# Kernel optimization log

Hardware: AMD Instinct MI355X
Metric: run time of the kernel (lower is better)

## Reference

```python
import jax, jax.numpy as jnp
import numpy as np
import math

B, L = 2048, 60
D, H, NL = 80, 8, 3
HD = D // H            # head_dim = 10
NLOC, NUSR = 1187, 46
DFF = 2 * D
IN_DIM = D + 24 + 32 + 2   # loc(80)+user(24)+weekday(16)+hour(16)+2 continuous


def _ln(x, g, b):
    m = jnp.mean(x, -1, keepdims=True)
    v = jnp.mean((x - m) ** 2, -1, keepdims=True)
    return (x - m) * jax.lax.rsqrt(v + 1e-5) * g + b


def setup_inputs():
    key = jax.random.key(0)
    k = lambda i: jax.random.fold_in(key, i)
    g = lambda i, shp, s: jax.random.normal(k(i), shp, dtype=jnp.float32) * s
    inp = {
        "loc_seq": jax.random.randint(k(0), (B, L), 0, NLOC),
        "user_seq": jax.random.randint(k(1), (B, L), 0, NUSR),
        "weekday_seq": jax.random.randint(k(2), (B, L), 0, 8),
        "start_min_seq": jax.random.randint(k(3), (B, L), 0, 1440),
        "dur_seq": jax.random.randint(k(4), (B, L), 0, 600),
        "diff_seq": jax.random.randint(k(5), (B, L), 0, 100),
        "seq_len": jax.random.randint(k(6), (B,), 1, L + 1),
    }
    # embedding tables (padding_idx=0 rows zeroed where the module uses it)
    inp["loc_table"] = g(10, (NLOC, D), 0.02).at[0].set(0.0)
    inp["user_table"] = g(11, (NUSR, 24), 0.02).at[0].set(0.0)
    inp["wk_table"] = g(12, (8, 16), 0.02).at[0].set(0.0)
    inp["hr_table"] = g(13, (25, 16), 0.02)
    inp["in_w"] = g(14, (IN_DIM, D), 0.09)
    inp["in_b"] = jnp.zeros((D,), jnp.float32)
    inp["in_g"] = jnp.ones((D,), jnp.float32)
    inp["in_be"] = jnp.zeros((D,), jnp.float32)
    inp["pos_emb"] = g(15, (1, L, D), 0.02)
    # per-layer stacked params (NL=3 layers)
    inp["qkv_w"] = g(16, (NL, D, 3 * D), 0.09)
    inp["proj_w"] = g(17, (NL, D, D), 0.11)
    inp["proj_b"] = jnp.zeros((NL, D), jnp.float32)
    inp["rel_emb"] = g(18, (NL, 2 * L - 1, HD), 1.0)
    inp["n1_g"] = jnp.ones((NL, D), jnp.float32)
    inp["n1_b"] = jnp.zeros((NL, D), jnp.float32)
    inp["ffn_w1"] = g(19, (NL, D, DFF), 0.09)
    inp["ffn_b1"] = jnp.zeros((NL, DFF), jnp.float32)
    inp["ffn_w2"] = g(20, (NL, DFF, D), 0.09)
    inp["ffn_b2"] = jnp.zeros((NL, D), jnp.float32)
    inp["n2_g"] = jnp.ones((NL, D), jnp.float32)
    inp["n2_b"] = jnp.zeros((NL, D), jnp.float32)
    inp["fn_g"] = jnp.ones((D,), jnp.float32)
    inp["fn_b"] = jnp.zeros((D,), jnp.float32)
    inp["pr_w1"] = g(21, (D, D), 0.11)
    inp["pr_b1"] = jnp.zeros((D,), jnp.float32)
    inp["pr_w2"] = g(22, (D, NLOC), 0.04)
    inp["pr_b2"] = jnp.zeros((NLOC,), jnp.float32)
    inp["protos"] = g(23, (NLOC, D), 0.04)
    inp["temp"] = jnp.asarray(2.0, jnp.float32)
    return inp


def reference(loc_seq, user_seq, weekday_seq, start_min_seq, dur_seq, diff_seq, seq_len,
              loc_table, user_table, wk_table, hr_table, in_w, in_b, in_g, in_be, pos_emb,
              qkv_w, proj_w, proj_b, rel_emb, n1_g, n1_b, ffn_w1, ffn_b1, ffn_w2, ffn_b2,
              n2_g, n2_b, fn_g, fn_b, pr_w1, pr_b1, pr_w2, pr_b2, protos, temp):
    Bx, Lx = loc_seq.shape
    loc_e = loc_table[loc_seq]                                            # [B,L,80]
    user_e = jnp.broadcast_to(user_table[user_seq[:, 0]][:, None, :], (Bx, Lx, 24))
    hour = jnp.clip(start_min_seq // 60, 0, 23)
    cont = jnp.stack([diff_seq.astype(jnp.float32) / 10.0,
                      dur_seq.astype(jnp.float32) / 300.0], -1)           # [B,L,2]
    x = jnp.concatenate([loc_e, user_e, wk_table[weekday_seq], hr_table[hour], cont], -1)
    x = _ln(x @ in_w + in_b, in_g, in_be) + pos_emb[:, :Lx, :]
    key_mask = loc_seq == 0                                               # mask keys [B,L]
    pos_idx = jnp.arange(Lx)[None, :] - jnp.arange(Lx)[:, None] + (Lx - 1)  # [L,L]
    scale = 1.0 / math.sqrt(HD)
    for l in range(NL):
        qkv = (x @ qkv_w[l]).reshape(Bx, Lx, 3, H, HD)
        q = qkv[:, :, 0].transpose(0, 2, 1, 3)                            # [B,H,L,hd]
        kk = qkv[:, :, 1].transpose(0, 2, 1, 3)
        v = qkv[:, :, 2].transpose(0, 2, 1, 3)
        rel = rel_emb[l][pos_idx]                                         # [L,L,hd]
        attn = (jnp.einsum('bhid,bhjd->bhij', q, kk)
                + jnp.einsum('bhid,ijd->bhij', q, rel)) * scale
        attn = jnp.where(key_mask[:, None, None, :], -jnp.inf, attn)
        a = jax.nn.softmax(attn, -1)
        o = jnp.einsum('bhij,bhjd->bhid', a, v).transpose(0, 2, 1, 3).reshape(Bx, Lx, D)
        x = _ln(x + o @ proj_w[l] + proj_b[l], n1_g[l], n1_b[l])
        f = jax.nn.gelu(x @ ffn_w1[l] + ffn_b1[l], approximate=False) @ ffn_w2[l] + ffn_b2[l]
        x = _ln(x + f, n2_g[l], n2_b[l])
    x = _ln(x, fn_g, fn_b)
    final = x[jnp.arange(Bx), jnp.clip(seq_len - 1, 0, Lx - 1)]           # [B,80]
    logits_param = jax.nn.gelu(final @ pr_w1 + pr_b1, approximate=False) @ pr_w2 + pr_b2
    fnorm = final / jnp.maximum(jnp.linalg.norm(final, axis=-1, keepdims=True), 1e-12)
    pnorm = protos / jnp.maximum(jnp.linalg.norm(protos, axis=-1, keepdims=True), 1e-12)
    logits = 0.5 * logits_param + 0.5 * (fnorm @ pnorm.T) * 15.0
    return logits / jnp.clip(temp, 0.5, 3.0)
```

## Files before the change

### kernel.cpp

```cpp
#include <hip/hip_runtime.h>
#include <hip/hip_bf16.h>
#include <math.h>

#define BB   2048
#define LL   60
#define DD   80
#define HH   8
#define HDD  10
#define NLNUM 3
#define NLOC 1187
#define DFF  160
#define IN_DIM 138
#define RELN 119
#define SCS  68
#define XP   21
#define HP   41
#define VP   35
#define TS   65

__device__ __forceinline__ float gelu_f(float a) {
  float x = fabsf(a) * 0.70710678118654752f;
  float t = 1.0f / (1.0f + 0.3275911f * x);
  float y = t * (0.254829592f + t * (-0.284496736f + t * (1.421413741f +
            t * (-1.453152027f + t * 1.061405429f))));
  float e = 1.0f - y * __expf(-x * x);
  float erf_s = copysignf(e, a);
  return 0.5f * a * (1.0f + erf_s);
}

__global__ __launch_bounds__(256) void k_rprep(
    const float* __restrict__ rel_emb, float* __restrict__ relTg) {
  int idx = blockIdx.x * 256 + threadIdx.x;
  if (idx >= 3600) return;
  int p = idx % 120;
  int d = (idx / 120) % 10;
  int l = idx / 1200;
  float v = 0.0f;
  if (p < RELN) v = rel_emb[l * RELN * HDD + p * HDD + d];
  relTg[idx] = v;
}

__global__ __launch_bounds__(256) void k_embed(
    const int* __restrict__ loc_seq, const int* __restrict__ user_seq,
    const int* __restrict__ wk_seq, const int* __restrict__ sm_seq,
    const int* __restrict__ dur_seq, const int* __restrict__ diff_seq,
    const float* __restrict__ loc_table, const float* __restrict__ user_table,
    const float* __restrict__ wk_table, const float* __restrict__ hr_table,
    const float* __restrict__ in_w, const float* __restrict__ in_b,
    const float* __restrict__ in_g, const float* __restrict__ in_be,
    const float* __restrict__ pos_emb, float* __restrict__ x) {
  int tok0 = blockIdx.x * 48, tid = threadIdx.x;
  __shared__ __align__(16) float vin[48 * VP * 4];
  __shared__ __align__(16) float ws[140 * 80];
  __shared__ float mstd[96];

  float4* vin4 = (float4*)vin;
  float4* ws4  = (float4*)ws;

  for (int i = tid; i < 140 * 20; i += 256) {
    int r = i / 20, c = i % 20;
    float4 v = make_float4(0.0f, 0.0f, 0.0f, 0.0f);
    if (r < IN_DIM) v = *(const float4*)(in_w + r * 80 + c * 4);
    ws4[i] = v;
  }
  for (int i = tid; i < 48 * 35; i += 256) {
    int t = i / 35, s = i % 35;
    int tok = tok0 + t;
    float4 v;
    if (s < 20) {
      int loc = loc_seq[tok];
      v = *(const float4*)(loc_table + (size_t)loc * 80 + s * 4);
    } else if (s < 26) {
      int usr = user_seq[(tok / LL) * LL];
      v = *(const float4*)(user_table + usr * 24 + (s - 20) * 4);
    } else if (s < 30) {
      int wk = wk_seq[tok];
      v = *(const float4*)(wk_table + wk * 16 + (s - 26) * 4);
    } else if (s < 34) {
      int hr = sm_seq[tok] / 60; hr = min(max(hr, 0), 23);
      v = *(const float4*)(hr_table + hr * 16 + (s - 30) * 4);
    } else {
      v.x = (float)diff_seq[tok] / 10.0f;
      v.y = (float)dur_seq[tok] / 300.0f;
      v.z = 0.0f; v.w = 0.0f;
    }
    vin4[t * VP + s] = v;
  }
  __syncthreads();

  int tg = tid / 20, cg = tid % 20, t0 = tg * 4;
  float acc[4][4] = {};
  if (tid < 240) {
    #pragma unroll 7
    for (int iq = 0; iq < 35; iq++) {
      float4 xv[4], wv[4];
      #pragma unroll
      for (int dt = 0; dt < 4; dt++) xv[dt] = vin4[(t0 + dt) * VP + iq];
      #pragma unroll
      for (int di = 0; di < 4; di++) wv[di] = ws4[(iq * 4 + di) * 20 + cg];
      #pragma unroll
      for (int dt = 0; dt < 4; dt++) {
        const float* xp = (const float*)&xv[dt];
        #pragma unroll
        for (int di = 0; di < 4; di++) {
          const float* wp = (const float*)&wv[di];
          #pragma unroll
          for (int dc = 0; dc < 4; dc++) acc[dt][dc] += xp[di] * wp[dc];
        }
      }
    }
  }
  __syncthreads();
  if (tid < 240) {
    float4 bb = *(const float4*)(in_b + cg * 4);
    const float* bp = (const float*)&bb;
    #pragma unroll
    for (int dt = 0; dt < 4; dt++) {
      float4 y;
      y.x = acc[dt][0] + bp[0];
      y.y = acc[dt][1] + bp[1];
      y.z = acc[dt][2] + bp[2];
      y.w = acc[dt][3] + bp[3];
      vin4[(t0 + dt) * VP + cg] = y;
    }
  }
  __syncthreads();
  if (tid < 48) {
    float s = 0.0f, s2 = 0.0f;
    #pragma unroll
    for (int iq = 0; iq < 20; iq++) {
      float4 v = vin4[tid * VP + iq];
      s  += v.x + v.y + v.z + v.w;
      s2 += v.x * v.x + v.y * v.y + v.z * v.z + v.w * v.w;
    }
    float mean = s / 80.0f;
    float var  = fmaxf(s2 / 80.0f - mean * mean, 0.0f);
    mstd[tid] = mean; mstd[48 + tid] = rsqrtf(var + 1e-5f);
  }
  __syncthreads();
  for (int e = tid; e < 960; e += 256) {
    int t = e / 20, c4 = e % 20;
    float4 v = vin4[t * VP + c4];
    float4 gg = *(const float4*)(in_g + c4 * 4);
    float4 bb = *(const float4*)(in_be + c4 * 4);
    float4 pe = *(const float4*)(pos_emb + ((tok0 + t) % LL) * 80 + c4 * 4);
    float m = mstd[t], r = mstd[48 + t];
    float4 out;
    out.x = (v.x - m) * r * gg.x + bb.x + pe.x;
    out.y = (v.y - m) * r * gg.y + bb.y + pe.y;
    out.z = (v.z - m) * r * gg.z + bb.z + pe.z;
    out.w = (v.w - m) * r * gg.w + bb.w + pe.w;
    ((float4*)(x + (size_t)tok0 * 80))[e] = out;
  }
}

__global__ __launch_bounds__(256) void k_qkv(
    const float* __restrict__ x, const float* __restrict__ qkv_w,
    float* __restrict__ qkvo) {
  int b = blockIdx.x, tid = threadIdx.x;
  __shared__ __align__(16) float xsT[20 * TS * 4];
  __shared__ __align__(16) float ws[80 * 60];

  const float4* xb4 = (const float4*)(x + (size_t)b * 4800);
  float4* xsT4 = (float4*)xsT;
  float4* ws4  = (float4*)ws;
  for (int i = tid; i < 1200; i += 256) {
    int t = i / 20, iq = i % 20;
    xsT4[iq * TS + t] = xb4[i];
  }

  for (int c0 = 0; c0 < 240; c0 += 60) {
    __syncthreads();
    for (int i = tid; i < 1200; i += 256)
      ws4[i] = *(const float4*)(qkv_w + (i / 15) * 240 + c0 + (i % 15) * 4);
    __syncthreads();
    if (tid < 225) {
      int tg = tid % 15, cg = tid / 15;
      int t0 = tg * 4;
      float acc[4][4] = {};
      #pragma unroll 5
      for (int iq = 0; iq < 20; iq++) {
        float4 xv[4], wv[4];
        #pragma unroll
        for (int dt = 0; dt < 4; dt++) xv[dt] = xsT4[iq * TS + t0 + dt];
        #pragma unroll
        for (int di = 0; di < 4; di++) wv[di] = ws4[(iq * 4 + di) * 15 + cg];
        #pragma unroll
        for (int dt = 0; dt < 4; dt++) {
          const float* xp = (const float*)&xv[dt];
          #pragma unroll
          for (int di = 0; di < 4; di++) {
            const float* wp = (const float*)&wv[di];
            #pragma unroll
            for (int dc = 0; dc < 4; dc++) acc[dt][dc] += xp[di] * wp[dc];
          }
        }
      }
      float* qb = qkvo + (size_t)b * 14400 + (size_t)(c0 + cg * 4) * 60 + t0;
      #pragma unroll
      for (int dc = 0; dc < 4; dc++)
        *(float4*)(qb + dc * 60) =
            make_float4(acc[0][dc], acc[1][dc], acc[2][dc], acc[3][dc]);
    }
  }
}

__global__ __launch_bounds__(256) void k_attn(
    const float* __restrict__ qkvo, const int* __restrict__ loc_seq,
    const float* __restrict__ relTg,
    float* __restrict__ o) {
  int bh = blockIdx.x;
  int b = bh >> 3, h = bh & 7;
  int tid = threadIdx.x;

  __shared__ __align__(16) float qs[HDD * 60];
  __shared__ __align__(16) float ks[HDD * 60];
  __shared__ __align__(16) float vs[HDD * 60];
  __shared__ __align__(16) float relT[HDD * 120];
  __shared__ __align__(16) float sc[60 * SCS];
  __shared__ __align__(16) float rsum[64];
  __shared__ float msk[60];

  const float4* src = (const float4*)(qkvo + (size_t)b * 14400);
  float4* q4 = (float4*)qs; float4* k4 = (float4*)ks; float4* v4 = (float4*)vs;
  for (int i = tid; i < 150; i += 256) {
    q4[i] = src[h * 150 + i];
    k4[i] = src[1200 + h * 150 + i];
    v4[i] = src[2400 + h * 150 + i];
  }
  const float4* rg4 = (const float4*)relTg;
  float4* relT4 = (float4*)relT;
  for (int i = tid; i < 300; i += 256) relT4[i] = rg4[i];
  if (tid < 60) msk[tid] = (loc_seq[b * LL + tid] == 0) ? 1.0f : 0.0f;
  __syncthreads();

  if (tid < 225) {
    int ig = tid / 15, jg = tid % 15;
    int i0 = ig * 4, j0 = jg * 4;
    int w0 = j0 - i0 + 56;
    float acc[4][4] = {};
    #pragma unroll
    for (int d = 0; d < 10; d++) {
      float4 qv = *(const float4*)(qs + d * 60 + i0);
      float4 kv = *(const float4*)(ks + d * 60 + j0);
      float4 rA = *(const float4*)(relT + d * 120 + w0);
      float4 rB = *(const float4*)(relT + d * 120 + w0 + 4);
      float rr[8] = {rA.x, rA.y, rA.z, rA.w, rB.x, rB.y, rB.z, rB.w};
      const float* qp = (const float*)&qv;
      const float* kp = (const float*)&kv;
      #pragma unroll
      for (int di = 0; di < 4; di++)
        #pragma unroll
        for (int dj = 0; dj < 4; dj++)
          acc[di][dj] += qp[di] * (kp[dj] + rr[dj - di + 3]);
    }
    const float scale = 0.31622776601683794f;
    #pragma unroll
    for (int di = 0; di < 4; di++) {
      #pragma unroll
      for (int dj = 0; dj < 4; dj++) {
        float v = acc[di][dj] * scale;
        if (msk[j0 + dj] != 0.0f) v = -1e30f;
        acc[di][dj] = v;
      }
      *(float4*)(sc + (i0 + di) * SCS + j0) =
          make_float4(acc[di][0], acc[di][1], acc[di][2], acc[di][3]);
    }
  }
  __syncthreads();

  if (tid < 60) {
    float* row = sc + tid * SCS;
    int c = (tid >> 3) & 7;
    float m0 = -3.0e38f, m1 = -3.0e38f, m2 = -3.0e38f, m3 = -3.0e38f;
    #pragma unroll
    for (int s = 0; s < 15; s++) {
      int k = c + s; if (k >= 15) k -= 15;
      float4 v = *(const float4*)(row + 4 * k);
      m0 = fmaxf(m0, v.x); m1 = fmaxf(m1, v.y);
      m2 = fmaxf(m2, v.z); m3 = fmaxf(m3, v.w);
    }
    float m = fmaxf(fmaxf(m0, m1), fmaxf(m2, m3));
    float s0 = 0.0f, s1 = 0.0f, s2 = 0.0f, s3 = 0.0f;
    #pragma unroll
    for (int s = 0; s < 15; s++) {
      int k = c + s; if (k >= 15) k -= 15;
      float4 v = *(float4*)(row + 4 * k);
      v.x = __expf(v.x - m); v.y = __expf(v.y - m);
      v.z = __expf(v.z - m); v.w = __expf(v.w - m);
      *(float4*)(row + 4 * k) = v;
      s0 += v.x; s1 += v.y; s2 += v.z; s3 += v.w;
    }
    rsum[tid] = 1.0f / (s0 + s1 + s2 + s3);
  }
  __syncthreads();

  if (tid < 150) {
    int ig = tid / 10, d = tid % 10;
    float acc[4] = {0, 0, 0, 0};
    #pragma unroll 5
    for (int jq = 0; jq < 15; jq++) {
      float4 vv = *(const float4*)(vs + d * 60 + jq * 4);
      #pragma unroll
      for (int di = 0; di < 4; di++) {
        float4 av = *(const float4*)(sc + (ig + 15 * di) * SCS + jq * 4);
        acc[di] += av.x * vv.x + av.y * vv.y + av.z * vv.z + av.w * vv.w;
      }
    }
    #pragma unroll
    for (int di = 0; di < 4; di++) {
      float r = rsum[ig + 15 * di];
      o[((size_t)b * 60 + ig + 15 * di) * 80 + h * 10 + d] = acc[di] * r;
    }
  }
}

__global__ __launch_bounds__(256) void k_pffn(
    const float* __restrict__ o, const float* __restrict__ proj_w,
    const float* __restrict__ proj_b, const float* __restrict__ g1,
    const float* __restrict__ be1,
    const float* __restrict__ w1, const float* __restrict__ b1,
    const float* __restrict__ w2, const float* __restrict__ b2,
    const float* __restrict__ g2, const float* __restrict__ be2,
    float* __restrict__ x) {
  int tok0 = blockIdx.x * 48, tid = threadIdx.x;
  __shared__ __align__(16) float ys[48 * XP * 4];
  __shared__ __align__(16) float hs[48 * HP * 4];
  __shared__ __align__(16) float ws[80 * 80];
  __shared__ float mstd[96];

  float4* ys4 = (float4*)ys;
  float4* hs4 = (float4*)hs;
  float4* os4 = (float4*)hs;
  float4* ws4 = (float4*)ws;

  const float4* ob4 = (const float4*)(o + (size_t)tok0 * 80);
  for (int i = tid; i < 960; i += 256) os4[(i / 20) * XP + (i % 20)] = ob4[i];
  for (int i = tid; i < 1600; i += 256)
    ws4[i] = *(const float4*)(proj_w + (i / 20) * 80 + (i % 20) * 4);
  __syncthreads();

  int tg = tid / 20, cg = tid % 20, t0 = tg * 4;
  {
    float acc[4][4] = {};
    if (tid < 240) {
      #pragma unroll
      for (int iq = 0; iq < 20; iq++) {
        float4 xv[4], wv[4];
        #pragma unroll
        for (int dt = 0; dt < 4; dt++) xv[dt] = os4[(t0 + dt) * XP + iq];
        #pragma unroll
        for (int di = 0; di < 4; di++) wv[di] = ws4[(iq * 4 + di) * 20 + cg];
        #pragma unroll
        for (int dt = 0; dt < 4; dt++) {
          const float* xp = (const float*)&xv[dt];
          #pragma unroll
          for (int di = 0; di < 4; di++) {
            const float* wp = (const float*)&wv[di];
            #pragma unroll
            for (int dc = 0; dc < 4; dc++) acc[dt][dc] += xp[di] * wp[dc];
          }
        }
      }
      float4 pb = *(const float4*)(proj_b + cg * 4);
      const float* pbp = (const float*)&pb;
      #pragma unroll
      for (int dt = 0; dt < 4; dt++) {
        float4 xr = *(const float4*)(x + (size_t)(tok0 + t0 + dt) * 80 + cg * 4);
        const float* xrp = (const float*)&xr;
        float4 out;
        out.x = acc[dt][0] + pbp[0] + xrp[0];
        out.y = acc[dt][1] + pbp[1] + xrp[1];
        out.z = acc[dt][2] + pbp[2] + xrp[2];
        out.w = acc[dt][3] + pbp[3] + xrp[3];
        ys4[(t0 + dt) * XP + cg] = out;
      }
    }
  }
  __syncthreads();
  if (tid < 48) {
    float s = 0.0f, s2 = 0.0f;
    #pragma unroll
    for (int iq = 0; iq < 20; iq++) {
      float4 v = ys4[tid * XP + iq];
      s  += v.x + v.y + v.z + v.w;
      s2 += v.x * v.x + v.y * v.y + v.z * v.z + v.w * v.w;
    }
    float mean = s / 80.0f;
    float var  = fmaxf(s2 / 80.0f - mean * mean, 0.0f);
    mstd[tid] = mean; mstd[48 + tid] = rsqrtf(var + 1e-5f);
  }
  __syncthreads();
  for (int e = tid; e < 960; e += 256) {
    int t = e / 20, c4 = e % 20;
    float4 v = ys4[t * XP + c4];
    float4 gg = *(const float4*)(g1 + c4 * 4);
    float4 bb = *(const float4*)(be1 + c4 * 4);
    float m = mstd[t], r = mstd[48 + t];
    v.x = (v.x - m) * r * gg.x + bb.x;
    v.y = (v.y - m) * r * gg.y + bb.y;
    v.z = (v.z - m) * r * gg.z + bb.z;
    v.w = (v.w - m) * r * gg.w + bb.w;
    ys4[t * XP + c4] = v;
  }

  for (int c0 = 0; c0 < 160; c0 += 80) {
    __syncthreads();
    for (int i = tid; i < 1600; i += 256)
      ws4[i] = *(const float4*)(w1 + (i / 20) * 160 + c0 + (i % 20) * 4);
    __syncthreads();
    if (tid < 240) {
      float acc[4][4] = {};
      #pragma unroll
      for (int iq = 0; iq < 20; iq++) {
        float4 xv[4], wv[4];
        #pragma unroll
        for (int dt = 0; dt < 4; dt++) xv[dt] = ys4[(t0 + dt) * XP + iq];
        #pragma unroll
        for (int di = 0; di < 4; di++) wv[di] = ws4[(iq * 4 + di) * 20 + cg];
        #pragma unroll
        for (int dt = 0; dt < 4; dt++) {
          const float* xp = (const float*)&xv[dt];
          #pragma unroll
          for (int di = 0; di < 4; di++) {
            const float* wp = (const float*)&wv[di];
            #pragma unroll
            for (int dc = 0; dc < 4; dc++) acc[dt][dc] += xp[di] * wp[dc];
          }
        }
      }
      float4 bb = *(const float4*)(b1 + c0 + cg * 4);
      const float* bp = (const float*)&bb;
      #pragma unroll
      for (int dt = 0; dt < 4; dt++) {
        float4 out;
        float* op = (float*)&out;
        #pragma unroll
        for (int dc = 0; dc < 4; dc++)
          op[dc] = gelu_f(acc[dt][dc] + bp[dc]);
        hs4[(t0 + dt) * HP + c0 / 4 + cg] = out;
      }
    }
  }

  float acc[4][4] = {};
  for (int k0 = 0; k0 < 160; k0 += 80) {
    __syncthreads();
    for (int i = tid; i < 1600; i += 256)
      ws4[i] = *(const float4*)(w2 + (size_t)(k0 + i / 20) * 80 + (i % 20) * 4);
    __syncthreads();
    if (tid < 240) {
      #pragma unroll
      for (int iq = 0; iq < 20; iq++) {
        float4 hv[4], wv[4];
        #pragma unroll
        for (int dt = 0; dt < 4; dt++) hv[dt] = hs4[(t0 + dt) * HP + k0 / 4 + iq];
        #pragma unroll
        for (int di = 0; di < 4; di++) wv[di] = ws4[(iq * 4 + di) * 20 + cg];
        #pragma unroll
        for (int dt = 0; dt < 4; dt++) {
          const float* hp = (const float*)&hv[dt];
          #pragma unroll
          for (int di = 0; di < 4; di++) {
            const float* wp = (const float*)&wv[di];
            #pragma unroll
            for (int dc = 0; dc < 4; dc++) acc[dt][dc] += hp[di] * wp[dc];
          }
        }
      }
    }
  }
  __syncthreads();
  if (tid < 240) {
    float4 bb = *(const float4*)(b2 + cg * 4);
    const float* bp = (const float*)&bb;
    #pragma unroll
    for (int dt = 0; dt < 4; dt++) {
      float4 xr = ys4[(t0 + dt) * XP + cg];
      const float* xrp = (const float*)&xr;
      float4 out;
      out.x = acc[dt][0] + bp[0] + xrp[0];
      out.y = acc[dt][1] + bp[1] + xrp[1];
      out.z = acc[dt][2] + bp[2] + xrp[2];
      out.w = acc[dt][3] + bp[3] + xrp[3];
      hs4[(t0 + dt) * HP + cg] = out;
    }
  }
  __syncthreads();
  if (tid < 48) {
    float s = 0.0f, s2 = 0.0f;
    #pragma unroll
    for (int iq = 0; iq < 20; iq++) {
      float4 v = hs4[tid * HP + iq];
      s  += v.x + v.y + v.z + v.w;
      s2 += v.x * v.x + v.y * v.y + v.z * v.z + v.w * v.w;
    }
    float mean = s / 80.0f;
    float var  = fmaxf(s2 / 80.0f - mean * mean, 0.0f);
    mstd[tid] = mean; mstd[48 + tid] = rsqrtf(var + 1e-5f);
  }
  __syncthreads();
  for (int e = tid; e < 960; e += 256) {
    int t = e / 20, c4 = e % 20;
    float4 v = hs4[t * HP + c4];
    float4 gg = *(const float4*)(g2 + c4 * 4);
    float4 bb = *(const float4*)(be2 + c4 * 4);
    float m = mstd[t], r = mstd[48 + t];
    float4 out;
    out.x = (v.x - m) * r * gg.x + bb.x;
    out.y = (v.y - m) * r * gg.y + bb.y;
    out.z = (v.z - m) * r * gg.z + bb.z;
    out.w = (v.w - m) * r * gg.w + bb.w;
    ((float4*)(x + (size_t)tok0 * 80))[e] = out;
  }
}

__global__ __launch_bounds__(128) void k_final(
    const float* __restrict__ x, const int* __restrict__ seq_len,
    const float* __restrict__ fn_g, const float* __restrict__ fn_b,
    const float* __restrict__ pr_w1, const float* __restrict__ pr_b1,
    float* __restrict__ fnorm, float* __restrict__ h1) {
  int b = blockIdx.x, tid = threadIdx.x;
  __shared__ float red[128], red2[128];
  __shared__ float fbuf[DD];
  int t = seq_len[b] - 1; t = min(max(t, 0), LL - 1);
  float v = 0.0f;
  if (tid < DD) v = x[((size_t)b * LL + t) * DD + tid];
  red[tid]  = (tid < DD) ? v : 0.0f;
  red2[tid] = (tid < DD) ? v * v : 0.0f;
  __syncthreads();
  for (int s = 64; s > 0; s >>= 1) {
    if (tid < s) { red[tid] += red[tid + s]; red2[tid] += red2[tid + s]; }
    __syncthreads();
  }
  float mean = red[0] / DD;
  float var  = fmaxf(red2[0] / DD - mean * mean, 0.0f);
  float rstd = rsqrtf(var + 1e-5f);
  float f = 0.0f;
  if (tid < DD) { f = (v - mean) * rstd * fn_g[tid] + fn_b[tid]; fbuf[tid] = f; }
  __syncthreads();
  red[tid] = (tid < DD) ? f * f : 0.0f;
  __syncthreads();
  for (int s = 64; s > 0; s >>= 1) {
    if (tid < s) red[tid] += red[tid + s];
    __syncthreads();
  }
  float rn = 1.0f / fmaxf(sqrtf(red[0]), 1e-12f);
  if (tid < DD) {
    fnorm[(size_t)b * DD + tid] = f * rn;
    float gacc = pr_b1[tid];
    for (int i = 0; i < DD; i++) gacc += fbuf[i] * pr_w1[i * DD + tid];
    h1[(size_t)b * DD + tid] = gelu_f(gacc);
  }
}

__global__ __launch_bounds__(128) void k_pnorm(
    const float* __restrict__ protos, float* __restrict__ pnormT) {
  int c = blockIdx.x, tid = threadIdx.x;
  __shared__ float red[128];
  float v = 0.0f;
  if (tid < DD) v = protos[(size_t)c * DD + tid];
  red[tid] = (tid < DD) ? v * v : 0.0f;
  __syncthreads();
  for (int s = 64; s > 0; s >>= 1) {
    if (tid < s) red[tid] += red[tid + s];
    __syncthreads();
  }
  float rn = 1.0f / fmaxf(sqrtf(red[0]), 1e-12f);
  if (tid < DD) pnormT[(size_t)tid * NLOC + c] = v * rn;
}

__global__ __launch_bounds__(256) void k_logits(
    const float* __restrict__ h1, const float* __restrict__ fnorm,
    const float* __restrict__ pr_w2, const float* __restrict__ pr_b2,
    const float* __restrict__ pnormT, const float* __restrict__ temp,
    float* __restrict__ out) {
  int b0 = (blockIdx.x / 5) * 4, cb = blockIdx.x % 5;
  int tid = threadIdx.x;
  int c = cb * 256 + tid;
  __shared__ float h1s[4][DD], fns[4][DD];
  for (int i = tid; i < 4 * DD; i += 256) {
    int j = i / DD, k = i % DD;
    h1s[j][k] = h1[(size_t)(b0 + j) * DD + k];
    fns[j][k] = fnorm[(size_t)(b0 + j) * DD + k];
  }
  __syncthreads();
  if (c < NLOC) {
    float a1[4] = {0, 0, 0, 0}, a2[4] = {0, 0, 0, 0};
    for (int k = 0; k < DD; k++) {
      float w = pr_w2[(size_t)k * NLOC + c];
      float p = pnormT[(size_t)k * NLOC + c];
      #pragma unroll
      for (int j = 0; j < 4; j++) {
        a1[j] += h1s[j][k] * w;
        a2[j] += fns[j][k] * p;
      }
    }
    float pb = pr_b2[c];
    float tt = fminf(fmaxf(temp[0], 0.5f), 3.0f);
    #pragma unroll
    for (int j = 0; j < 4; j++)
      out[(size_t)(b0 + j) * NLOC + c] = (0.5f * (a1[j] + pb) + 7.5f * a2[j]) / tt;
  }
}

extern "C" void kernel_launch(void* const* d_in, const int* in_sizes, int n_in,
                              void* d_out, int out_size, void* d_ws, size_t ws_size,
                              hipStream_t stream) {
  const int* loc_seq   = (const int*)d_in[0];
  const int* user_seq  = (const int*)d_in[1];
  const int* wk_seq    = (const int*)d_in[2];
  const int* sm_seq    = (const int*)d_in[3];
  const int* dur_seq   = (const int*)d_in[4];
  const int* diff_seq  = (const int*)d_in[5];
  const int* seq_len   = (const int*)d_in[6];
  const float* loc_table = (const float*)d_in[7];
  const float* user_table= (const float*)d_in[8];
  const float* wk_table  = (const float*)d_in[9];
  const float* hr_table  = (const float*)d_in[10];
  const float* in_w   = (const float*)d_in[11];
  const float* in_b   = (const float*)d_in[12];
  const float* in_g   = (const float*)d_in[13];
  const float* in_be  = (const float*)d_in[14];
  const float* pos_emb= (const float*)d_in[15];
  const float* qkv_w  = (const float*)d_in[16];
  const float* proj_w = (const float*)d_in[17];
  const float* proj_b = (const float*)d_in[18];
  const float* rel_emb= (const float*)d_in[19];
  const float* n1_g   = (const float*)d_in[20];
  const float* n1_b   = (const float*)d_in[21];
  const float* ffn_w1 = (const float*)d_in[22];
  const float* ffn_b1 = (const float*)d_in[23];
  const float* ffn_w2 = (const float*)d_in[24];
  const float* ffn_b2 = (const float*)d_in[25];
  const float* n2_g   = (const float*)d_in[26];
  const float* n2_b   = (const float*)d_in[27];
  const float* fn_g   = (const float*)d_in[28];
  const float* fn_b   = (const float*)d_in[29];
  const float* pr_w1  = (const float*)d_in[30];
  const float* pr_b1  = (const float*)d_in[31];
  const float* pr_w2  = (const float*)d_in[32];
  const float* pr_b2  = (const float*)d_in[33];
  const float* protos = (const float*)d_in[34];
  const float* temp   = (const float*)d_in[35];
  float* out = (float*)d_out;

  float* x      = (float*)d_ws;
  float* o      = x + (size_t)BB * LL * DD;
  float* qkvo   = o + (size_t)BB * LL * DD;
  float* fnorm  = qkvo + (size_t)BB * 14400;
  float* h1     = fnorm + (size_t)BB * DD;
  float* pnormT = h1 + (size_t)BB * DD;
  float* relTg  = pnormT + (size_t)DD * NLOC;

  k_rprep<<<15, 256, 0, stream>>>(rel_emb, relTg);

  k_embed<<<BB * LL / 48, 256, 0, stream>>>(loc_seq, user_seq, wk_seq, sm_seq,
                                            dur_seq, diff_seq, loc_table,
                                            user_table, wk_table, hr_table,
                                            in_w, in_b, in_g, in_be, pos_emb, x);

  for (int l = 0; l < NLNUM; l++) {
    k_qkv<<<BB, 256, 0, stream>>>(x, qkv_w + (size_t)l * 80 * 240, qkvo);
    k_attn<<<BB * HH, 256, 0, stream>>>(qkvo, loc_seq,
                                        relTg + (size_t)l * 1200, o);
    k_pffn<<<BB * LL / 48, 256, 0, stream>>>(
        o, proj_w + (size_t)l * DD * DD, proj_b + (size_t)l * DD,
        n1_g + (size_t)l * DD, n1_b + (size_t)l * DD,
        ffn_w1 + (size_t)l * DD * DFF, ffn_b1 + (size_t)l * DFF,
        ffn_w2 + (size_t)l * DFF * DD, ffn_b2 + (size_t)l * DD,
        n2_g + (size_t)l * DD, n2_b + (size_t)l * DD, x);
  }

  k_pnorm<<<NLOC, 128, 0, stream>>>(protos, pnormT);
  k_final<<<BB, 128, 0, stream>>>(x, seq_len, fn_g, fn_b, pr_w1, pr_b1, fnorm, h1);
  k_logits<<<(BB / 4) * 5, 256, 0, stream>>>(h1, fnorm, pr_w2, pr_b2, pnormT, temp, out);
}
```

Measured before the change: 1.520 ms.

## Switch embed, QKV and FFN kernels to one-token-per-thread register GEMMs

Rewrites k_embed, k_qkv and k_pffn so each thread owns one token and keeps its full 80-wide row in registers. Weights are read directly from global memory with uniform (broadcast) indices instead of being staged through shared memory, which removes all __syncthreads and the LDS tiling. Launch grids change to 256 tokens per block, or 4 batches per block for QKV. The cost is very high register pressure from 80-160 float arrays, which risks spills and low occupancy. Every thread also redundantly streams the whole weight matrix through the scalar/L1 path, and the strided per-thread stores in k_qkv are uncoalesced.

```diff
diff --git a/kernel.cpp b/kernel.cpp
--- a/kernel.cpp
+++ b/kernel.cpp
@@ -13,10 +13,10 @@
 #define IN_DIM 138
 #define RELN 119
 #define SCS  68
-#define XP   21
-#define HP   41
-#define VP   35
-#define TS   65
+
+#define ACC4(A, base, S, W)                                                  \
+  { (A)[(base)] += (S) * (W).x; (A)[(base) + 1] += (S) * (W).y;              \
+    (A)[(base) + 2] += (S) * (W).z; (A)[(base) + 3] += (S) * (W).w; }
 
 __device__ __forceinline__ float gelu_f(float a) {
   float x = fabsf(a) * 0.70710678118654752f;
@@ -49,158 +49,153 @@
     const float* __restrict__ in_w, const float* __restrict__ in_b,
     const float* __restrict__ in_g, const float* __restrict__ in_be,
     const float* __restrict__ pos_emb, float* __restrict__ x) {
-  int tok0 = blockIdx.x * 48, tid = threadIdx.x;
-  __shared__ __align__(16) float vin[48 * VP * 4];
-  __shared__ __align__(16) float ws[140 * 80];
-  __shared__ float mstd[96];
-
-  float4* vin4 = (float4*)vin;
-  float4* ws4  = (float4*)ws;
-
-  for (int i = tid; i < 140 * 20; i += 256) {
-    int r = i / 20, c = i % 20;
-    float4 v = make_float4(0.0f, 0.0f, 0.0f, 0.0f);
-    if (r < IN_DIM) v = *(const float4*)(in_w + r * 80 + c * 4);
-    ws4[i] = v;
-  }
-  for (int i = tid; i < 48 * 35; i += 256) {
-    int t = i / 35, s = i % 35;
-    int tok = tok0 + t;
-    float4 v;
-    if (s < 20) {
-      int loc = loc_seq[tok];
-      v = *(const float4*)(loc_table + (size_t)loc * 80 + s * 4);
-    } else if (s < 26) {
-      int usr = user_seq[(tok / LL) * LL];
-      v = *(const float4*)(user_table + usr * 24 + (s - 20) * 4);
-    } else if (s < 30) {
-      int wk = wk_seq[tok];
-      v = *(const float4*)(wk_table + wk * 16 + (s - 26) * 4);
-    } else if (s < 34) {
-      int hr = sm_seq[tok] / 60; hr = min(max(hr, 0), 23);
-      v = *(const float4*)(hr_table + hr * 16 + (s - 30) * 4);
-    } else {
-      v.x = (float)diff_seq[tok] / 10.0f;
-      v.y = (float)dur_seq[tok] / 300.0f;
-      v.z = 0.0f; v.w = 0.0f;
-    }
-    vin4[t * VP + s] = v;
-  }
-  __syncthreads();
-
-  int tg = tid / 20, cg = tid % 20, t0 = tg * 4;
-  float acc[4][4] = {};
-  if (tid < 240) {
-    #pragma unroll 7
-    for (int iq = 0; iq < 35; iq++) {
-      float4 xv[4], wv[4];
-      #pragma unroll
-      for (int dt = 0; dt < 4; dt++) xv[dt] = vin4[(t0 + dt) * VP + iq];
-      #pragma unroll
-      for (int di = 0; di < 4; di++) wv[di] = ws4[(iq * 4 + di) * 20 + cg];
-      #pragma unroll
-      for (int dt = 0; dt < 4; dt++) {
-        const float* xp = (const float*)&xv[dt];
-        #pragma unroll
-        for (int di = 0; di < 4; di++) {
-          const float* wp = (const float*)&wv[di];
-          #pragma unroll
-          for (int dc = 0; dc < 4; dc++) acc[dt][dc] += xp[di] * wp[dc];
-        }
-      }
-    }
-  }
-  __syncthreads();
-  if (tid < 240) {
-    float4 bb = *(const float4*)(in_b + cg * 4);
-    const float* bp = (const float*)&bb;
-    #pragma unroll
-    for (int dt = 0; dt < 4; dt++) {
-      float4 y;
-      y.x = acc[dt][0] + bp[0];
-      y.y = acc[dt][1] + bp[1];
-      y.z = acc[dt][2] + bp[2];
-      y.w = acc[dt][3] + bp[3];
-      vin4[(t0 + dt) * VP + cg] = y;
-    }
-  }
-  __syncthreads();
-  if (tid < 48) {
-    float s = 0.0f, s2 = 0.0f;
-    #pragma unroll
-    for (int iq = 0; iq < 20; iq++) {
-      float4 v = vin4[tid * VP + iq];
-      s  += v.x + v.y + v.z + v.w;
-      s2 += v.x * v.x + v.y * v.y + v.z * v.z + v.w * v.w;
-    }
-    float mean = s / 80.0f;
-    float var  = fmaxf(s2 / 80.0f - mean * mean, 0.0f);
-    mstd[tid] = mean; mstd[48 + tid] = rsqrtf(var + 1e-5f);
-  }
-  __syncthreads();
-  for (int e = tid; e < 960; e += 256) {
-    int t = e / 20, c4 = e % 20;
-    float4 v = vin4[t * VP + c4];
-    float4 gg = *(const float4*)(in_g + c4 * 4);
-    float4 bb = *(const float4*)(in_be + c4 * 4);
-    float4 pe = *(const float4*)(pos_emb + ((tok0 + t) % LL) * 80 + c4 * 4);
-    float m = mstd[t], r = mstd[48 + t];
-    float4 out;
-    out.x = (v.x - m) * r * gg.x + bb.x + pe.x;
-    out.y = (v.y - m) * r * gg.y + bb.y + pe.y;
-    out.z = (v.z - m) * r * gg.z + bb.z + pe.z;
-    out.w = (v.w - m) * r * gg.w + bb.w + pe.w;
-    ((float4*)(x + (size_t)tok0 * 80))[e] = out;
+  int g = blockIdx.x * 256 + threadIdx.x;
+  int b = g / LL, t = g - b * LL;
+  int loc = loc_seq[g];
+  int usr = user_seq[b * LL];
+  int wk  = wk_seq[g];
+  int hr  = min(max(sm_seq[g] / 60, 0), 23);
+  const float4* w4 = (const float4*)in_w;
+
+  float acc[DD];
+  {
+    const float4* bb4 = (const float4*)in_b;
+    #pragma unroll
+    for (int c4 = 0; c4 < 20; c4++) {
+      float4 v = bb4[c4];
+      acc[c4 * 4] = v.x; acc[c4 * 4 + 1] = v.y;
+      acc[c4 * 4 + 2] = v.z; acc[c4 * 4 + 3] = v.w;
+    }
+  }
+
+  const float4* le4 = (const float4*)(loc_table + (size_t)loc * DD);
+  for (int iq = 0; iq < 20; iq++) {
+    float4 xv = le4[iq];
+    const float* xp = (const float*)&xv;
+    #pragma unroll
+    for (int dk = 0; dk < 4; dk++) {
+      float s = xp[dk];
+      #pragma unroll
+      for (int c4 = 0; c4 < 20; c4++) {
+        float4 wv = w4[(iq * 4 + dk) * 20 + c4];
+        ACC4(acc, c4 * 4, s, wv)
+      }
+    }
+  }
+  const float4* ue4 = (const float4*)(user_table + usr * 24);
+  #pragma unroll
+  for (int iq = 0; iq < 6; iq++) {
+    float4 xv = ue4[iq];
+    const float* xp = (const float*)&xv;
+    #pragma unroll
+    for (int dk = 0; dk < 4; dk++) {
+      float s = xp[dk];
+      #pragma unroll
+      for (int c4 = 0; c4 < 20; c4++) {
+        float4 wv = w4[(80 + iq * 4 + dk) * 20 + c4];
+        ACC4(acc, c4 * 4, s, wv)
+      }
+    }
+  }
+  const float4* we4 = (const float4*)(wk_table + wk * 16);
+  #pragma unroll
+  for (int iq = 0; iq < 4; iq++) {
+    float4 xv = we4[iq];
+    const float* xp = (const float*)&xv;
+    #pragma unroll
+    for (int dk = 0; dk < 4; dk++) {
+      float s = xp[dk];
+      #pragma unroll
+      for (int c4 = 0; c4 < 20; c4++) {
+        float4 wv = w4[(104 + iq * 4 + dk) * 20 + c4];
+        ACC4(acc, c4 * 4, s, wv)
+      }
+    }
+  }
+  const float4* he4 = (const float4*)(hr_table + hr * 16);
+  #pragma unroll
+  for (int iq = 0; iq < 4; iq++) {
+    float4 xv = he4[iq];
+    const float* xp = (const float*)&xv;
+    #pragma unroll
+    for (int dk = 0; dk < 4; dk++) {
+      float s = xp[dk];
+      #pragma unroll
+      for (int c4 = 0; c4 < 20; c4++) {
+        float4 wv = w4[(120 + iq * 4 + dk) * 20 + c4];
+        ACC4(acc, c4 * 4, s, wv)
+      }
+    }
+  }
+  {
+    float xd = (float)diff_seq[g] * 0.1f;
+    float xu = (float)dur_seq[g] * (1.0f / 300.0f);
+    #pragma unroll
+    for (int c4 = 0; c4 < 20; c4++) {
+      float4 wa = w4[136 * 20 + c4];
+      float4 wb = w4[137 * 20 + c4];
+      acc[c4 * 4]     += xd * wa.x + xu * wb.x;
+      acc[c4 * 4 + 1] += xd * wa.y + xu * wb.y;
+      acc[c4 * 4 + 2] += xd * wa.z + xu * wb.z;
+      acc[c4 * 4 + 3] += xd * wa.w + xu * wb.w;
+    }
+  }
+
+  float s1 = 0.0f, s2 = 0.0f;
+  #pragma unroll
+  for (int c = 0; c < DD; c++) { s1 += acc[c]; s2 += acc[c] * acc[c]; }
+  float m = s1 * 0.0125f;
+  float var = fmaxf(s2 * 0.0125f - m * m, 0.0f);
+  float r = rsqrtf(var + 1e-5f);
+
+  const float4* g4  = (const float4*)in_g;
+  const float4* be4 = (const float4*)in_be;
+  const float4* pe4 = (const float4*)(pos_emb + t * DD);
+  float4* xo4 = (float4*)(x + (size_t)g * DD);
+  #pragma unroll
+  for (int c4 = 0; c4 < 20; c4++) {
+    float4 gv = g4[c4], bv = be4[c4], pv = pe4[c4];
+    float4 ov;
+    ov.x = (acc[c4 * 4]     - m) * r * gv.x + bv.x + pv.x;
+    ov.y = (acc[c4 * 4 + 1] - m) * r * gv.y + bv.y + pv.y;
+    ov.z = (acc[c4 * 4 + 2] - m) * r * gv.z + bv.z + pv.z;
+    ov.w = (acc[c4 * 4 + 3] - m) * r * gv.w + bv.w + pv.w;
+    xo4[c4] = ov;
   }
 }
 
 __global__ __launch_bounds__(256) void k_qkv(
     const float* __restrict__ x, const float* __restrict__ qkv_w,
     float* __restrict__ qkvo) {
-  int b = blockIdx.x, tid = threadIdx.x;
-  __shared__ __align__(16) float xsT[20 * TS * 4];
-  __shared__ __align__(16) float ws[80 * 60];
-
-  const float4* xb4 = (const float4*)(x + (size_t)b * 4800);
-  float4* xsT4 = (float4*)xsT;
-  float4* ws4  = (float4*)ws;
-  for (int i = tid; i < 1200; i += 256) {
-    int t = i / 20, iq = i % 20;
-    xsT4[iq * TS + t] = xb4[i];
-  }
-
-  for (int c0 = 0; c0 < 240; c0 += 60) {
-    __syncthreads();
-    for (int i = tid; i < 1200; i += 256)
-      ws4[i] = *(const float4*)(qkv_w + (i / 15) * 240 + c0 + (i % 15) * 4);
-    __syncthreads();
-    if (tid < 225) {
-      int tg = tid % 15, cg = tid / 15;
-      int t0 = tg * 4;
-      float acc[4][4] = {};
-      #pragma unroll 5
-      for (int iq = 0; iq < 20; iq++) {
-        float4 xv[4], wv[4];
+  int tid = threadIdx.x;
+  int b = blockIdx.x * 4 + (tid >> 6);
+  int t = tid & 63;
+  int tt = min(t, 59);
+  const float4* xr4 = (const float4*)(x + ((size_t)b * LL + tt) * DD);
+  const float4* w4  = (const float4*)qkv_w;
+  float* ob = qkvo + (size_t)b * 14400 + t;
+
+  for (int c0 = 0; c0 < 240; c0 += 80) {
+    float acc[DD];
+    #pragma unroll
+    for (int c = 0; c < DD; c++) acc[c] = 0.0f;
+    int cq0 = c0 >> 2;
+    for (int iq = 0; iq < 20; iq++) {
+      float4 xv = xr4[iq];
+      const float* xp = (const float*)&xv;
+      #pragma unroll
+      for (int dk = 0; dk < 4; dk++) {
+        float s = xp[dk];
         #pragma unroll
-        for (int dt = 0; dt < 4; dt++) xv[dt] = xsT4[iq * TS + t0 + dt];
-        #pragma unroll
-        for (int di = 0; di < 4; di++) wv[di] = ws4[(iq * 4 + di) * 15 + cg];
-        #pragma unroll
-        for (int dt = 0; dt < 4; dt++) {
-          const float* xp = (const float*)&xv[dt];
-          #pragma unroll
-          for (int di = 0; di < 4; di++) {
-            const float* wp = (const float*)&wv[di];
-            #pragma unroll
-            for (int dc = 0; dc < 4; dc++) acc[dt][dc] += xp[di] * wp[dc];
-          }
+        for (int c4 = 0; c4 < 20; c4++) {
+          float4 wv = w4[(iq * 4 + dk) * 60 + cq0 + c4];
+          ACC4(acc, c4 * 4, s, wv)
         }
       }
-      float* qb = qkvo + (size_t)b * 14400 + (size_t)(c0 + cg * 4) * 60 + t0;
-      #pragma unroll
-      for (int dc = 0; dc < 4; dc++)
-        *(float4*)(qb + dc * 60) =
-            make_float4(acc[0][dc], acc[1][dc], acc[2][dc], acc[3][dc]);
+    }
+    if (t < 60) {
+      #pragma unroll
+      for (int c = 0; c < DD; c++) ob[(size_t)(c0 + c) * 60] = acc[c];
     }
   }
 }
@@ -323,195 +318,119 @@
     const float* __restrict__ w2, const float* __restrict__ b2,
     const float* __restrict__ g2, const float* __restrict__ be2,
     float* __restrict__ x) {
-  int tok0 = blockIdx.x * 48, tid = threadIdx.x;
-  __shared__ __align__(16) float ys[48 * XP * 4];
-  __shared__ __align__(16) float hs[48 * HP * 4];
-  __shared__ __align__(16) float ws[80 * 80];
-  __shared__ float mstd[96];
-
-  float4* ys4 = (float4*)ys;
-  float4* hs4 = (float4*)hs;
-  float4* os4 = (float4*)hs;
-  float4* ws4 = (float4*)ws;
-
-  const float4* ob4 = (const float4*)(o + (size_t)tok0 * 80);
-  for (int i = tid; i < 960; i += 256) os4[(i / 20) * XP + (i % 20)] = ob4[i];
-  for (int i = tid; i < 1600; i += 256)
-    ws4[i] = *(const float4*)(proj_w + (i / 20) * 80 + (i % 20) * 4);
-  __syncthreads();
-
-  int tg = tid / 20, cg = tid % 20, t0 = tg * 4;
+  int g = blockIdx.x * 256 + threadIdx.x;
+  const float4* or4 = (const float4*)(o + (size_t)g * DD);
+  float4* xr4 = (float4*)(x + (size_t)g * DD);
+  const float4* pw4 = (const float4*)proj_w;
+  const float4* w14 = (const float4*)w1;
+  const float4* w24 = (const float4*)w2;
+
+  float y[DD];
   {
-    float acc[4][4] = {};
-    if (tid < 240) {
-      #pragma unroll
-      for (int iq = 0; iq < 20; iq++) {
-        float4 xv[4], wv[4];
+    float acc[DD];
+    #pragma unroll
+    for (int c = 0; c < DD; c++) acc[c] = 0.0f;
+    for (int iq = 0; iq < 20; iq++) {
+      float4 xv = or4[iq];
+      const float* xp = (const float*)&xv;
+      #pragma unroll
+      for (int dk = 0; dk < 4; dk++) {
+        float s = xp[dk];
         #pragma unroll
-        for (int dt = 0; dt < 4; dt++) xv[dt] = os4[(t0 + dt) * XP + iq];
-        #pragma unroll
-        for (int di = 0; di < 4; di++) wv[di] = ws4[(iq * 4 + di) * 20 + cg];
-        #pragma unroll
-        for (int dt = 0; dt < 4; dt++) {
-          const float* xp = (const float*)&xv[dt];
-          #pragma unroll
-          for (int di = 0; di < 4; di++) {
-            const float* wp = (const float*)&wv[di];
-            #pragma unroll
-            for (int dc = 0; dc < 4; dc++) acc[dt][dc] += xp[di] * wp[dc];
-          }
+        for (int c4 = 0; c4 < 20; c4++) {
+          float4 wv = pw4[(iq * 4 + dk) * 20 + c4];
+          ACC4(acc, c4 * 4, s, wv)
         }
       }
-      float4 pb = *(const float4*)(proj_b + cg * 4);
-      const float* pbp = (const float*)&pb;
-      #pragma unroll
-      for (int dt = 0; dt < 4; dt++) {
-        float4 xr = *(const float4*)(x + (size_t)(tok0 + t0 + dt) * 80 + cg * 4);
-        const float* xrp = (const float*)&xr;
-        float4 out;
-        out.x = acc[dt][0] + pbp[0] + xrp[0];
-        out.y = acc[dt][1] + pbp[1] + xrp[1];
-        out.z = acc[dt][2] + pbp[2] + xrp[2];
-        out.w = acc[dt][3] + pbp[3] + xrp[3];
-        ys4[(t0 + dt) * XP + cg] = out;
-      }
-    }
-  }
-  __syncthreads();
-  if (tid < 48) {
-    float s = 0.0f, s2 = 0.0f;
-    #pragma unroll
-    for (int iq = 0; iq < 20; iq++) {
-      float4 v = ys4[tid * XP + iq];
-      s  += v.x + v.y + v.z + v.w;
-      s2 += v.x * v.x + v.y * v.y + v.z * v.z + v.w * v.w;
-    }
-    float mean = s / 80.0f;
-    float var  = fmaxf(s2 / 80.0f - mean * mean, 0.0f);
-    mstd[tid] = mean; mstd[48 + tid] = rsqrtf(var + 1e-5f);
-  }
-  __syncthreads();
-  for (int e = tid; e < 960; e += 256) {
-    int t = e / 20, c4 = e % 20;
-    float4 v = ys4[t * XP + c4];
-    float4 gg = *(const float4*)(g1 + c4 * 4);
-    float4 bb = *(const float4*)(be1 + c4 * 4);
-    float m = mstd[t], r = mstd[48 + t];
-    v.x = (v.x - m) * r * gg.x + bb.x;
-    v.y = (v.y - m) * r * gg.y + bb.y;
-    v.z = (v.z - m) * r * gg.z + bb.z;
-    v.w = (v.w - m) * r * gg.w + bb.w;
-    ys4[t * XP + c4] = v;
-  }
-
-  for (int c0 = 0; c0 < 160; c0 += 80) {
-    __syncthreads();
-    for (int i = tid; i < 1600; i += 256)
-      ws4[i] = *(const float4*)(w1 + (i / 20) * 160 + c0 + (i % 20) * 4);
-    __syncthreads();
-    if (tid < 240) {
-      float acc[4][4] = {};
-      #pragma unroll
-      for (int iq = 0; iq < 20; iq++) {
-        float4 xv[4], wv[4];
-        #pragma unroll
-        for (int dt = 0; dt < 4; dt++) xv[dt] = ys4[(t0 + dt) * XP + iq];
-        #pragma unroll
-        for (int di = 0; di < 4; di++) wv[di] = ws4[(iq * 4 + di) * 20 + cg];
-        #pragma unroll
-        for (int dt = 0; dt < 4; dt++) {
-          const float* xp = (const float*)&xv[dt];
-          #pragma unroll
-          for (int di = 0; di < 4; di++) {
-            const float* wp = (const float*)&wv[di];
-            #pragma unroll
-            for (int dc = 0; dc < 4; dc++) acc[dt][dc] += xp[di] * wp[dc];
-          }
-        }
-      }
-      float4 bb = *(const float4*)(b1 + c0 + cg * 4);
-      const float* bp = (const float*)&bb;
-      #pragma unroll
-      for (int dt = 0; dt < 4; dt++) {
-        float4 out;
-        float* op = (float*)&out;
-        #pragma unroll
-        for (int dc = 0; dc < 4; dc++)
-          op[dc] = gelu_f(acc[dt][dc] + bp[dc]);
-        hs4[(t0 + dt) * HP + c0 / 4 + cg] = out;
-      }
-    }
-  }
-
-  float acc[4][4] = {};
-  for (int k0 = 0; k0 < 160; k0 += 80) {
-    __syncthreads();
-    for (int i = tid; i < 1600; i += 256)
-      ws4[i] = *(const float4*)(w2 + (size_t)(k0 + i / 20) * 80 + (i % 20) * 4);
-    __syncthreads();
-    if (tid < 240) {
-      #pragma unroll
-      for (int iq = 0; iq < 20; iq++) {
-        float4 hv[4], wv[4];
-        #pragma unroll
-        for (int dt = 0; dt < 4; dt++) hv[dt] = hs4[(t0 + dt) * HP + k0 / 4 + iq];
-        #pragma unroll
-        for (int di = 0; di < 4; di++) wv[di] = ws4[(iq * 4 + di) * 20 + cg];
-        #pragma unroll
-        for (int dt = 0; dt < 4; dt++) {
-          const float* hp = (const float*)&hv[dt];
-          #pragma unroll
-          for (int di = 0; di < 4; di++) {
-            const float* wp = (const float*)&wv[di];
-            #pragma unroll
-            for (int dc = 0; dc < 4; dc++) acc[dt][dc] += hp[di] * wp[dc];
-          }
-        }
-      }
-    }
-  }
-  __syncthreads();
-  if (tid < 240) {
-    float4 bb = *(const float4*)(b2 + cg * 4);
-    const float* bp = (const float*)&bb;
-    #pragma unroll
-    for (int dt = 0; dt < 4; dt++) {
-      float4 xr = ys4[(t0 + dt) * XP + cg];
-      const float* xrp = (const float*)&xr;
-      float4 out;
-      out.x = acc[dt][0] + bp[0] + xrp[0];
-      out.y = acc[dt][1] + bp[1] + xrp[1];
-      out.z = acc[dt][2] + bp[2] + xrp[2];
-      out.w = acc[dt][3] + bp[3] + xrp[3];
-      hs4[(t0 + dt) * HP + cg] = out;
-    }
-  }
-  __syncthreads();
-  if (tid < 48) {
-    float s = 0.0f, s2 = 0.0f;
-    #pragma unroll
-    for (int iq = 0; iq < 20; iq++) {
-      float4 v = hs4[tid * HP + iq];
-      s  += v.x + v.y + v.z + v.w;
-      s2 += v.x * v.x + v.y * v.y + v.z * v.z + v.w * v.w;
-    }
-    float mean = s / 80.0f;
-    float var  = fmaxf(s2 / 80.0f - mean * mean, 0.0f);
-    mstd[tid] = mean; mstd[48 + tid] = rsqrtf(var + 1e-5f);
-  }
-  __syncthreads();
-  for (int e = tid; e < 960; e += 256) {
-    int t = e / 20, c4 = e % 20;
-    float4 v = hs4[t * HP + c4];
-    float4 gg = *(const float4*)(g2 + c4 * 4);
-    float4 bb = *(const float4*)(be2 + c4 * 4);
-    float m = mstd[t], r = mstd[48 + t];
-    float4 out;
-    out.x = (v.x - m) * r * gg.x + bb.x;
-    out.y = (v.y - m) * r * gg.y + bb.y;
-    out.z = (v.z - m) * r * gg.z + bb.z;
-    out.w = (v.w - m) * r * gg.w + bb.w;
-    ((float4*)(x + (size_t)tok0 * 80))[e] = out;
+    }
+    float s1 = 0.0f, s2 = 0.0f;
+    #pragma unroll
+    for (int c4 = 0; c4 < 20; c4++) {
+      float4 pb = ((const float4*)proj_b)[c4];
+      float4 xv = xr4[c4];
+      float v0 = acc[c4 * 4]     + pb.x + xv.x;
+      float v1 = acc[c4 * 4 + 1] + pb.y + xv.y;
+      float v2 = acc[c4 * 4 + 2] + pb.z + xv.z;
+      float v3 = acc[c4 * 4 + 3] + pb.w + xv.w;
+      y[c4 * 4] = v0; y[c4 * 4 + 1] = v1; y[c4 * 4 + 2] = v2; y[c4 * 4 + 3] = v3;
+      s1 += v0 + v1 + v2 + v3;
+      s2 += v0 * v0 + v1 * v1 + v2 * v2 + v3 * v3;
+    }
+    float m = s1 * 0.0125f;
+    float var = fmaxf(s2 * 0.0125f - m * m, 0.0f);
+    float r = rsqrtf(var + 1e-5f);
+    #pragma unroll
+    for (int c4 = 0; c4 < 20; c4++) {
+      float4 gv = ((const float4*)g1)[c4];
+      float4 bv = ((const float4*)be1)[c4];
+      y[c4 * 4]     = (y[c4 * 4]     - m) * r * gv.x + bv.x;
+      y[c4 * 4 + 1] = (y[c4 * 4 + 1] - m) * r * gv.y + bv.y;
+      y[c4 * 4 + 2] = (y[c4 * 4 + 2] - m) * r * gv.z + bv.z;
+      y[c4 * 4 + 3] = (y[c4 * 4 + 3] - m) * r * gv.w + bv.w;
+    }
+  }
+
+  float out[DD];
+  #pragma unroll
+  for (int c = 0; c < DD; c++) out[c] = 0.0f;
+
+  for (int hc = 0; hc < 20; hc++) {
+    float hh[8];
+    {
+      float4 ba = ((const float4*)b1)[hc * 2];
+      float4 bb = ((const float4*)b1)[hc * 2 + 1];
+      hh[0] = ba.x; hh[1] = ba.y; hh[2] = ba.z; hh[3] = ba.w;
+      hh[4] = bb.x; hh[5] = bb.y; hh[6] = bb.z; hh[7] = bb.w;
+    }
+    #pragma unroll
+    for (int k = 0; k < DD; k++) {
+      float yv = y[k];
+      float4 wa = w14[k * 40 + hc * 2];
+      float4 wb = w14[k * 40 + hc * 2 + 1];
+      hh[0] += yv * wa.x; hh[1] += yv * wa.y;
+      hh[2] += yv * wa.z; hh[3] += yv * wa.w;
+      hh[4] += yv * wb.x; hh[5] += yv * wb.y;
+      hh[6] += yv * wb.z; hh[7] += yv * wb.w;
+    }
+    #pragma unroll
+    for (int j = 0; j < 8; j++) hh[j] = gelu_f(hh[j]);
+    #pragma unroll
+    for (int j = 0; j < 8; j++) {
+      float hv = hh[j];
+      #pragma unroll
+      for (int c4 = 0; c4 < 20; c4++) {
+        float4 wv = w24[(hc * 8 + j) * 20 + c4];
+        ACC4(out, c4 * 4, hv, wv)
+      }
+    }
+  }
+
+  float s1 = 0.0f, s2 = 0.0f;
+  #pragma unroll
+  for (int c4 = 0; c4 < 20; c4++) {
+    float4 bb = ((const float4*)b2)[c4];
+    float v0 = out[c4 * 4]     + bb.x + y[c4 * 4];
+    float v1 = out[c4 * 4 + 1] + bb.y + y[c4 * 4 + 1];
+    float v2 = out[c4 * 4 + 2] + bb.z + y[c4 * 4 + 2];
+    float v3 = out[c4 * 4 + 3] + bb.w + y[c4 * 4 + 3];
+    out[c4 * 4] = v0; out[c4 * 4 + 1] = v1;
+    out[c4 * 4 + 2] = v2; out[c4 * 4 + 3] = v3;
+    s1 += v0 + v1 + v2 + v3;
+    s2 += v0 * v0 + v1 * v1 + v2 * v2 + v3 * v3;
+  }
+  float m = s1 * 0.0125f;
+  float var = fmaxf(s2 * 0.0125f - m * m, 0.0f);
+  float r = rsqrtf(var + 1e-5f);
+  #pragma unroll
+  for (int c4 = 0; c4 < 20; c4++) {
+    float4 gv = ((const float4*)g2)[c4];
+    float4 bv = ((const float4*)be2)[c4];
+    float4 ov;
+    ov.x = (out[c4 * 4]     - m) * r * gv.x + bv.x;
+    ov.y = (out[c4 * 4 + 1] - m) * r * gv.y + bv.y;
+    ov.z = (out[c4 * 4 + 2] - m) * r * gv.z + bv.z;
+    ov.w = (out[c4 * 4 + 3] - m) * r * gv.w + bv.w;
+    xr4[c4] = ov;
   }
 }
 
@@ -655,16 +574,16 @@
 
   k_rprep<<<15, 256, 0, stream>>>(rel_emb, relTg);
 
-  k_embed<<<BB * LL / 48, 256, 0, stream>>>(loc_seq, user_seq, wk_seq, sm_seq,
-                                            dur_seq, diff_seq, loc_table,
-                                            user_table, wk_table, hr_table,
-                                            in_w, in_b, in_g, in_be, pos_emb, x);
+  k_embed<<<BB * LL / 256, 256, 0, stream>>>(loc_seq, user_seq, wk_seq, sm_seq,
+                                             dur_seq, diff_seq, loc_table,
+                                             user_table, wk_table, hr_table,
+                                             in_w, in_b, in_g, in_be, pos_emb, x);
 
   for (int l = 0; l < NLNUM; l++) {
-    k_qkv<<<BB, 256, 0, stream>>>(x, qkv_w + (size_t)l * 80 * 240, qkvo);
+    k_qkv<<<BB / 4, 256, 0, stream>>>(x, qkv_w + (size_t)l * 80 * 240, qkvo);
     k_attn<<<BB * HH, 256, 0, stream>>>(qkvo, loc_seq,
                                         relTg + (size_t)l * 1200, o);
-    k_pffn<<<BB * LL / 48, 256, 0, stream>>>(
+    k_pffn<<<BB * LL / 256, 256, 0, stream>>>(
         o, proj_w + (size_t)l * DD * DD, proj_b + (size_t)l * DD,
         n1_g + (size_t)l * DD, n1_b + (size_t)l * DD,
         ffn_w1 + (size_t)l * DD * DFF, ffn_b1 + (size_t)l * DFF,
```

After: 1.747 ms. 1.15x slower.
